# Kernel tuning notes

Measured on AMD Instinct MI355X. Metric: run time of the kernel, lower is better.

Reference implementation:

```python
import jax, jax.numpy as jnp
import numpy as np

NUM_HEADS = 12
HEAD_DIM = 64
SCALE = HEAD_DIM ** -0.5


def setup_inputs() -> dict:
    key = jax.random.key(0)
    ks = jax.random.split(key, 6)
    B, N, C = 32, 577, 768
    x = jax.random.normal(ks[0], (B, N, C), dtype=jnp.float32)
    w_qkv = jax.random.normal(ks[1], (3 * C, C), dtype=jnp.float32) * (C ** -0.5)
    w_proj = jax.random.normal(ks[2], (C, C), dtype=jnp.float32) * (C ** -0.5)
    b_proj = jnp.zeros((C,), dtype=jnp.float32)
    # RoPE tables for the N-1 patch tokens, per rotation pair (head_dim//2)
    ang = jax.random.uniform(ks[3], (N - 1, HEAD_DIM // 2), dtype=jnp.float32) * (2 * np.pi)
    cos = jnp.cos(ang)
    sin = jnp.sin(ang)
    return {"x": x, "w_qkv": w_qkv, "w_proj": w_proj, "b_proj": b_proj, "cos": cos, "sin": sin}


def _rotate(t, cos, sin):
    # t: [B,H,P,D]; cos/sin: [P,D/2] broadcast to [1,1,P,D/2]
    t1 = t[..., 0::2]
    t2 = t[..., 1::2]
    c = cos[None, None]
    s = sin[None, None]
    r1 = t1 * c - t2 * s
    r2 = t1 * s + t2 * c
    return jnp.stack([r1, r2], axis=-1).reshape(t.shape)


def reference(x, w_qkv, w_proj, b_proj, cos, sin):
    B, N, C = x.shape
    H, D = NUM_HEADS, HEAD_DIM
    qkv = (x @ w_qkv.T).reshape(B, N, 3, H, D)
    qkv = jnp.transpose(qkv, (2, 0, 3, 1, 4))  # [3,B,H,N,D]
    q, k, v = qkv[0], qkv[1], qkv[2]
    # RoPE on patch tokens only; CLS token (index 0) left unrotated
    q = jnp.concatenate([q[:, :, :1], _rotate(q[:, :, 1:], cos, sin)], axis=2)
    k = jnp.concatenate([k[:, :, :1], _rotate(k[:, :, 1:], cos, sin)], axis=2)
    attn = jnp.einsum("bhqd,bhkd->bhqk", q, k) * SCALE
    attn = jax.nn.softmax(attn, axis=-1)
    out = jnp.einsum("bhqk,bhkd->bhqd", attn, v)
    out = jnp.transpose(out, (0, 2, 1, 3)).reshape(B, N, C)
    return out @ w_proj.T + b_proj
```

## Files before the change

kernel.cpp:

```cpp
#include <hip/hip_runtime.h>


#define M_ROWS 18464
#define M_PAD  18560
#define CDIM   768
#define QKVN   2304
#define NHEADS 12
#define BHEADS 384
#define NSEQ   577
#define NPAD   640
#define SCALE  0.125f

typedef __bf16 bf16x8 __attribute__((ext_vector_type(8)));
typedef __bf16 bf16x4 __attribute__((ext_vector_type(4)));
typedef float  f32x4  __attribute__((ext_vector_type(4)));

typedef const __attribute__((address_space(1))) void* gas_ptr;
typedef __attribute__((address_space(3))) void* las_ptr;

__device__ inline void gload16(const __bf16* g, __bf16* l) {
  __builtin_amdgcn_global_load_lds((gas_ptr)g, (las_ptr)l, 16, 0, 0);
}

__device__ inline int xcd_swizzle(int orig, int nwg) {
  int q = nwg >> 3, r = nwg & 7;
  int xcd = orig & 7, idx = orig >> 3;
  int base = (xcd < r) ? xcd * (q + 1) : r * (q + 1) + (xcd - r) * q;
  return base + idx;
}


__global__ void cvt_pad(const float* __restrict__ src, __bf16* __restrict__ dst,
                        long n_src, long n_dst) {
  long i = ((long)blockIdx.x * 256 + threadIdx.x) * 4;
  if (i >= n_dst) return;
  if (i + 3 < n_src) {
    f32x4 v = *(const f32x4*)(src + i);
    bf16x4 o = {(__bf16)v[0], (__bf16)v[1], (__bf16)v[2], (__bf16)v[3]};
    *(bf16x4*)(dst + i) = o;
  } else {
#pragma unroll
    for (int j = 0; j < 4; j++)
      if (i + j < n_dst) dst[i + j] = (i + j < n_src) ? (__bf16)src[i + j] : (__bf16)0.0f;
  }
}

__global__ void pad_zero(__bf16* __restrict__ q, __bf16* __restrict__ k) {
  int i = blockIdx.x * 256 + threadIdx.x;
  if (i >= BHEADS * 63 * 64) return;
  int d = i & 63;
  int t = i >> 6;
  int sp = t % 63, bh = t / 63;
  int s = NSEQ + sp;
  q[((size_t)bh * NPAD + s) * 64 + d] = (__bf16)0.0f;
  k[((size_t)bh * NPAD + s) * 64 + d] = (__bf16)0.0f;
}


#define G1_NWG (18 * 145)

__launch_bounds__(256, 2)
__global__ void gemm1(const __bf16* __restrict__ A, const __bf16* __restrict__ Bw,
                      __bf16* __restrict__ qq, __bf16* __restrict__ kk,
                      __bf16* __restrict__ vr,
                      const float* __restrict__ cs, const float* __restrict__ sn) {
  __shared__ __bf16 smem[3 * 4096 * 2];
  const int wgid = xcd_swizzle(blockIdx.x, G1_NWG);
  const int bn = wgid % 18, bm = wgid / 18;
  const int tid = threadIdx.x;
  const int w = tid >> 6, lane = tid & 63;
  const int lr = lane & 15, quad = lane >> 4;
  const int r0 = tid >> 2;
  const int kq = (tid & 3) * 8;
  const int K = CDIM;

  f32x4 acc[4][4] = {};
  const __bf16* Ab = A + (size_t)(bm * 128 + r0) * K + kq;
  const __bf16* Bb = Bw + (size_t)(bn * 128 + r0) * K + kq;
  const int wm = (w >> 1) * 64, wn = (w & 1) * 64;

  auto stage = [&](int kt, int buf) __attribute__((always_inline)) {
    gload16(Ab + kt, &smem[buf * 4096 + tid * 8]);
    gload16(Ab + kt + 64 * K, &smem[buf * 4096 + tid * 8 + 2048]);
    gload16(Bb + kt, &smem[12288 + buf * 4096 + tid * 8]);
    gload16(Bb + kt + 64 * K, &smem[12288 + buf * 4096 + tid * 8 + 2048]);
  };

  stage(0, 0);
  stage(32, 1);
  asm volatile("s_waitcnt vmcnt(4)" ::: "memory");
  asm volatile("s_barrier" ::: "memory");

  int c0 = 0, c1 = 1, c2 = 2;
#pragma unroll 1
  for (int kt = 0; kt < K; kt += 32) {
    if (kt + 64 < K) stage(kt + 64, c2);

    bf16x8 af[4], bfr[4];
#pragma unroll
    for (int i = 0; i < 4; i++) {
      af[i]  = *(const bf16x8*)&smem[c0 * 4096 + (wm + i * 16 + lr) * 32 + quad * 8];
      bfr[i] = *(const bf16x8*)&smem[12288 + c0 * 4096 + (wn + i * 16 + lr) * 32 + quad * 8];
    }
#pragma unroll
    for (int i = 0; i < 4; i++)
#pragma unroll
      for (int j = 0; j < 4; j++)
        acc[i][j] = __builtin_amdgcn_mfma_f32_16x16x32_bf16(af[i], bfr[j], acc[i][j], 0, 0, 0);

    if (kt + 64 < K)      asm volatile("s_waitcnt vmcnt(4)" ::: "memory");
    else if (kt + 32 < K) asm volatile("s_waitcnt vmcnt(0)" ::: "memory");
    asm volatile("s_barrier" ::: "memory");

    int tmp = c0; c0 = c1; c1 = c2; c2 = tmp;
  }

  __syncthreads();
  __bf16* tile = smem;
  const bool isv = (bn >= 12);

#pragma unroll
  for (int i = 0; i < 4; i++) {
#pragma unroll
    for (int r = 0; r < 4; r++) {
      int ml = wm + i * 16 + quad * 4 + r;
      int m = bm * 128 + ml;
      int s = 0;
      if (!isv) { int b = m / NSEQ; s = m - b * NSEQ; }
#pragma unroll
      for (int j = 0; j < 4; j++) {
        int nl = wn + j * 16 + lr;
        float v = acc[i][j][r];
        float outv = v;
        if (!isv) {
          float pv = __shfl_xor(v, 1, 64);
          if (s >= 1 && m < M_ROWS) {
            int d = nl & 63;
            float c  = cs[(size_t)(s - 1) * 32 + (d >> 1)];
            float sv = sn[(size_t)(s - 1) * 32 + (d >> 1)];
            outv = (nl & 1) ? (pv * sv + v * c) : (v * c - pv * sv);
          }
        }
        tile[ml * 136 + nl] = (__bf16)outv;
      }
    }
  }
  __syncthreads();

  {
    const int tq = tid >> 4, tc = tid & 15;
    const int t_blk = bn / 6;
    const int bnq = bn % 6;
    __bf16* dstb = (t_blk == 0) ? qq : (t_blk == 1) ? kk : vr;
    const int SS = (t_blk == 2) ? NSEQ : NPAD;
    const int h = bnq * 2 + (tc >> 3);
    const int d0 = (tc & 7) * 8;
#pragma unroll
    for (int p = 0; p < 8; p++) {
      int ml = p * 16 + tq;
      int m = bm * 128 + ml;
      if (m < M_ROWS) {
        int b = m / NSEQ, s = m - b * NSEQ;
        bf16x8 val = *(const bf16x8*)&tile[ml * 136 + tc * 8];
        *(bf16x8*)&dstb[(((size_t)(b * NHEADS + h) * SS + s) << 6) + d0] = val;
      }
    }
  }
}


__global__ void vtrans(const __bf16* __restrict__ vr, __bf16* __restrict__ vt) {
  __shared__ __bf16 t[64 * 72];
  int blk = blockIdx.x;
  int bh = blk / 10, sc = blk % 10;
  int tid = threadIdx.x;
  int ts = tid >> 2;
  int dc = (tid & 3) * 16;
  int s = sc * 64 + ts;
  bf16x8 a = {}, b2 = {};
  if (s < NSEQ) {
    const __bf16* src = vr + ((size_t)bh * NSEQ + s) * 64 + dc;
    a  = *(const bf16x8*)src;
    b2 = *(const bf16x8*)(src + 8);
  }
#pragma unroll
  for (int e = 0; e < 8; e++) {
    t[(dc + e) * 72 + ts]     = a[e];
    t[(dc + 8 + e) * 72 + ts] = b2[e];
  }
  __syncthreads();
  int d = tid >> 2;
  int scol = (tid & 3) * 16;
  bf16x8 o0 = *(const bf16x8*)&t[d * 72 + scol];
  bf16x8 o1 = *(const bf16x8*)&t[d * 72 + scol + 8];
  __bf16* dst = vt + ((size_t)bh * 64 + d) * NPAD + sc * 64 + scol;
  *(bf16x8*)dst = o0;
  *(bf16x8*)(dst + 8) = o1;
}


#define AT_NWG (BHEADS * 5)

__launch_bounds__(256, 3)
__global__ void attn(const __bf16* __restrict__ q, const __bf16* __restrict__ k,
                     const __bf16* __restrict__ vT, __bf16* __restrict__ aoh) {
  __shared__ __bf16 KVs[2][8192];
  __shared__ float Xf[4][1152];
  const int blk = xcd_swizzle(blockIdx.x, AT_NWG);
  const int qt5 = blk % 5, bh = blk / 5;
  const int b = bh / NHEADS, h = bh % NHEADS;
  const int tid = threadIdx.x;
  const int w = tid >> 6, lane = tid & 63;
  const int lr = lane & 15, quad = lane >> 4;
  const int qbase = qt5 * 128 + w * 32;

  float* xw = &Xf[w][0];
  __bf16* pw = (__bf16*)xw;

  bf16x8 qf[2][2];
#pragma unroll
  for (int qt = 0; qt < 2; qt++)
#pragma unroll
    for (int kh = 0; kh < 2; kh++)
      qf[qt][kh] = *(const bf16x8*)(q + ((size_t)bh * NPAD + qbase + qt * 16 + lr) * 64 + kh * 32 + quad * 8);

  f32x4 O[2][4] = {};
  float l_p[2] = {0.0f, 0.0f};
  const float C1 = SCALE * 1.44269504089f;
  const float C0 = -8.0f * 1.44269504089f;
  const __bf16* kbase = k + (size_t)bh * NPAD * 64;
  const __bf16* vbase = vT + (size_t)bh * 64 * NPAD;

  const int sr0 = tid >> 3, sc0 = tid & 7;
  const int sr1 = (256 + tid) >> 3;
  const int cg0 = sc0 ^ (sr0 & 7);
  const int cg1 = sc0 ^ (sr1 & 7);
  auto stage = [&](int kv0, int buf) __attribute__((always_inline)) {
    gload16(kbase + (size_t)(kv0 + sr0) * 64 + cg0 * 8, &KVs[buf][tid * 8]);
    gload16(kbase + (size_t)(kv0 + sr1) * 64 + cg1 * 8, &KVs[buf][2048 + tid * 8]);
    gload16(vbase + (size_t)sr0 * NPAD + kv0 + cg0 * 8, &KVs[buf][4096 + tid * 8]);
    gload16(vbase + (size_t)sr1 * NPAD + kv0 + cg1 * 8, &KVs[buf][6144 + tid * 8]);
  };

  stage(0, 0);
  asm volatile("s_waitcnt vmcnt(0)" ::: "memory");
  asm volatile("s_barrier" ::: "memory");

  int cur = 0;
#pragma unroll 1
  for (int it = 0; it < 9; it++) {
    if (it < 8) stage((it + 1) * 64, cur ^ 1);

    bf16x8 kf[4][2];
#pragma unroll
    for (int nt = 0; nt < 4; nt++)
#pragma unroll
      for (int kh = 0; kh < 2; kh++)
        kf[nt][kh] = *(const bf16x8*)&KVs[cur][(nt * 16 + lr) * 64 + (((kh * 4 + quad) ^ (lr & 7)) * 8)];

    f32x4 st[2][4];
    __builtin_amdgcn_s_setprio(1);
#pragma unroll
    for (int qt = 0; qt < 2; qt++)
#pragma unroll
      for (int nt = 0; nt < 4; nt++) {
        f32x4 z = {};
        z = __builtin_amdgcn_mfma_f32_16x16x32_bf16(kf[nt][0], qf[qt][0], z, 0, 0, 0);
        z = __builtin_amdgcn_mfma_f32_16x16x32_bf16(kf[nt][1], qf[qt][1], z, 0, 0, 0);
        st[qt][nt] = z;
      }
    __builtin_amdgcn_s_setprio(0);

    bf16x8 vf[4][2];
#pragma unroll
    for (int nt2 = 0; nt2 < 4; nt2++)
#pragma unroll
      for (int kt = 0; kt < 2; kt++)
        vf[nt2][kt] = *(const bf16x8*)&KVs[cur][4096 + (nt2 * 16 + lr) * 64 + (((kt * 4 + quad) ^ (lr & 7)) * 8)];

#pragma unroll
    for (int qt = 0; qt < 2; qt++) {
      float rs = 0.0f;
#pragma unroll
      for (int nt = 0; nt < 4; nt++) {
        f32x4 pv;
#pragma unroll
        for (int r = 0; r < 4; r++)
          pv[r] = __builtin_amdgcn_exp2f(st[qt][nt][r] * C1 + C0);
        rs += pv[0] + pv[1] + pv[2] + pv[3];
        bf16x4 pk = {(__bf16)pv[0], (__bf16)pv[1], (__bf16)pv[2], (__bf16)pv[3]};
        *(bf16x4*)&pw[qt * 1152 + lr * 72 + nt * 16 + quad * 4] = pk;
      }
      l_p[qt] += rs;
    }

    bf16x8 pf[2][2];
#pragma unroll
    for (int qt = 0; qt < 2; qt++)
#pragma unroll
      for (int kt = 0; kt < 2; kt++)
        pf[qt][kt] = *(const bf16x8*)&pw[qt * 1152 + lr * 72 + kt * 32 + quad * 8];

    __builtin_amdgcn_s_setprio(1);
#pragma unroll
    for (int qt = 0; qt < 2; qt++)
#pragma unroll
      for (int nt2 = 0; nt2 < 4; nt2++) {
        O[qt][nt2] = __builtin_amdgcn_mfma_f32_16x16x32_bf16(vf[nt2][0], pf[qt][0], O[qt][nt2], 0, 0, 0);
        O[qt][nt2] = __builtin_amdgcn_mfma_f32_16x16x32_bf16(vf[nt2][1], pf[qt][1], O[qt][nt2], 0, 0, 0);
      }
    __builtin_amdgcn_s_setprio(0);

    asm volatile("s_waitcnt vmcnt(0)" ::: "memory");
    asm volatile("s_barrier" ::: "memory");
    cur ^= 1;
  }

  {
    bf16x8 k5[2];
#pragma unroll
    for (int kh = 0; kh < 2; kh++)
      k5[kh] = *(const bf16x8*)(kbase + (size_t)576 * 64 + kh * 32 + quad * 8);
    float p5[2];
#pragma unroll
    for (int qt = 0; qt < 2; qt++) {
      float s = 0.0f;
#pragma unroll
      for (int kh = 0; kh < 2; kh++)
#pragma unroll
        for (int j = 0; j < 8; j++)
          s += (float)qf[qt][kh][j] * (float)k5[kh][j];
      s += __shfl_xor(s, 16, 64);
      s += __shfl_xor(s, 32, 64);
      p5[qt] = __builtin_amdgcn_exp2f(s * C1 + C0);
      if (quad == 0) l_p[qt] += p5[qt];
    }
#pragma unroll
    for (int nt2 = 0; nt2 < 4; nt2++)
#pragma unroll
      for (int r = 0; r < 4; r++) {
        float vv = (float)vbase[(size_t)(nt2 * 16 + quad * 4 + r) * NPAD + 576];
        O[0][nt2][r] += p5[0] * vv;
        O[1][nt2][r] += p5[1] * vv;
      }
  }

#pragma unroll
  for (int qt = 0; qt < 2; qt++) {
    float lf = l_p[qt];
    lf += __shfl_xor(lf, 16, 64);
    lf += __shfl_xor(lf, 32, 64);
    float inv = 1.0f / lf;
#pragma unroll
    for (int nt2 = 0; nt2 < 4; nt2++) {
      f32x4 t;
#pragma unroll
      for (int r = 0; r < 4; r++) t[r] = O[qt][nt2][r] * inv;
      *(f32x4*)&xw[lr * 68 + nt2 * 16 + quad * 4] = t;
    }
#pragma unroll
    for (int p = 0; p < 4; p++) {
      int lm = p * 4 + quad;
      int s = qbase + qt * 16 + lm;
      if (s < NSEQ) {
        f32x4 t = *(const f32x4*)&xw[lm * 68 + lr * 4];
        bf16x4 hi;
#pragma unroll
        for (int r = 0; r < 4; r++) hi[r] = (__bf16)t[r];
        size_t base = ((size_t)b * NSEQ + s) * CDIM + h * 64 + lr * 4;
        *(bf16x4*)&aoh[base] = hi;
      }
    }
  }
}


#define G2_NWG (6 * 145)

__launch_bounds__(256, 2)
__global__ void gemm2(const __bf16* __restrict__ A, const __bf16* __restrict__ Bw,
                      const float* __restrict__ bias, float* __restrict__ out) {
  __shared__ __bf16 As[3][128 * 32];
  __shared__ __bf16 Bs[3][128 * 32];
  const int wgid = xcd_swizzle(blockIdx.x, G2_NWG);
  const int bn = wgid % 6, bm = wgid / 6;
  const int tid = threadIdx.x;
  const int w = tid >> 6, lane = tid & 63;
  const int lr = lane & 15, quad = lane >> 4;
  const int r0 = tid >> 2;
  const int kq = (tid & 3) * 8;
  const int K = CDIM;

  f32x4 acc[4][4] = {};
  const __bf16* Ab = A + (size_t)(bm * 128 + r0) * K + kq;
  const __bf16* Bb = Bw + (size_t)(bn * 128 + r0) * K + kq;
  const int wm = (w >> 1) * 64, wn = (w & 1) * 64;

  auto stage = [&](int kt, int buf) __attribute__((always_inline)) {
    gload16(Ab + kt, &As[buf][tid * 8]);
    gload16(Ab + kt + 64 * K, &As[buf][tid * 8 + 2048]);
    gload16(Bb + kt, &Bs[buf][tid * 8]);
    gload16(Bb + kt + 64 * K, &Bs[buf][tid * 8 + 2048]);
  };

  stage(0, 0);
  stage(32, 1);
  asm volatile("s_waitcnt vmcnt(4)" ::: "memory");
  asm volatile("s_barrier" ::: "memory");

  int c0 = 0, c1 = 1, c2 = 2;
#pragma unroll 1
  for (int kt = 0; kt < K; kt += 32) {
    if (kt + 64 < K) stage(kt + 64, c2);

    bf16x8 af[4], bfr[4];
#pragma unroll
    for (int i = 0; i < 4; i++) {
      af[i]  = *(const bf16x8*)&As[c0][(wm + i * 16 + lr) * 32 + quad * 8];
      bfr[i] = *(const bf16x8*)&Bs[c0][(wn + i * 16 + lr) * 32 + quad * 8];
    }
#pragma unroll
    for (int i = 0; i < 4; i++)
#pragma unroll
      for (int j = 0; j < 4; j++)
        acc[i][j] = __builtin_amdgcn_mfma_f32_16x16x32_bf16(af[i], bfr[j], acc[i][j], 0, 0, 0);

    if (kt + 64 < K)      asm volatile("s_waitcnt vmcnt(4)" ::: "memory");
    else if (kt + 32 < K) asm volatile("s_waitcnt vmcnt(0)" ::: "memory");
    asm volatile("s_barrier" ::: "memory");

    int tmp = c0; c0 = c1; c1 = c2; c2 = tmp;
  }

#pragma unroll
  for (int i = 0; i < 4; i++)
#pragma unroll
    for (int r = 0; r < 4; r++) {
      int m = bm * 128 + wm + i * 16 + quad * 4 + r;
      if (m < M_ROWS) {
#pragma unroll
        for (int j = 0; j < 4; j++) {
          int n = bn * 128 + wn + j * 16 + lr;
          out[(size_t)m * CDIM + n] = acc[i][j][r] + bias[n];
        }
      }
    }
}


extern "C" void kernel_launch(void* const* d_in, const int* in_sizes, int n_in,
                              void* d_out, int out_size, void* d_ws, size_t ws_size,
                              hipStream_t stream) {
  const float* x      = (const float*)d_in[0];
  const float* w_qkv  = (const float*)d_in[1];
  const float* w_proj = (const float*)d_in[2];
  const float* b_proj = (const float*)d_in[3];
  const float* cosp   = (const float*)d_in[4];
  const float* sinp   = (const float*)d_in[5];
  float* out = (float*)d_out;

  char* ws = (char*)d_ws;
  auto carve = [&](size_t elts) {
    __bf16* p = (__bf16*)ws;
    ws += ((elts * 2 + 255) / 256) * 256;
    return p;
  };
  __bf16* xb    = carve((size_t)M_PAD * CDIM);
  __bf16* wqkvb = carve((size_t)QKVN * CDIM);
  __bf16* wpb   = carve((size_t)CDIM * CDIM);
  __bf16* qq    = carve((size_t)BHEADS * NPAD * 64);
  __bf16* kk    = carve((size_t)BHEADS * NPAD * 64);
  __bf16* vv    = carve((size_t)BHEADS * NPAD * 64);
  __bf16* aoh   = carve((size_t)M_PAD * CDIM);
  __bf16* vr    = aoh;

  cvt_pad<<<((M_PAD * CDIM) / 4 + 255) / 256, 256, 0, stream>>>(x, xb, (long)M_ROWS * CDIM, (long)M_PAD * CDIM);
  cvt_pad<<<((QKVN * CDIM) / 4 + 255) / 256, 256, 0, stream>>>(w_qkv, wqkvb, (long)QKVN * CDIM, (long)QKVN * CDIM);
  cvt_pad<<<((CDIM * CDIM) / 4 + 255) / 256, 256, 0, stream>>>(w_proj, wpb, (long)CDIM * CDIM, (long)CDIM * CDIM);
  pad_zero<<<(BHEADS * 63 * 64 + 255) / 256, 256, 0, stream>>>(qq, kk);
  gemm1<<<G1_NWG, 256, 0, stream>>>(xb, wqkvb, qq, kk, vr, cosp, sinp);
  vtrans<<<BHEADS * 10, 256, 0, stream>>>(vr, vv);
  attn<<<AT_NWG, 256, 0, stream>>>(qq, kk, vv, aoh);
  gemm2<<<G2_NWG, 256, 0, stream>>>(aoh, wpb, b_proj, out);
}
```

Measured before the change: 355.6 us.

## Split attention block into 8 waves each owning 16 query rows

Result: no change. 357.2 us (+0.4%).

```diff
diff --git a/kernel.cpp b/kernel.cpp
--- a/kernel.cpp
+++ b/kernel.cpp
@@ -201,45 +201,39 @@
 
 #define AT_NWG (BHEADS * 5)
 
-__launch_bounds__(256, 3)
+__launch_bounds__(512, 2)
 __global__ void attn(const __bf16* __restrict__ q, const __bf16* __restrict__ k,
                      const __bf16* __restrict__ vT, __bf16* __restrict__ aoh) {
   __shared__ __bf16 KVs[2][8192];
-  __shared__ float Xf[4][1152];
+  __shared__ float Xf[8][1152];
   const int blk = xcd_swizzle(blockIdx.x, AT_NWG);
   const int qt5 = blk % 5, bh = blk / 5;
   const int b = bh / NHEADS, h = bh % NHEADS;
   const int tid = threadIdx.x;
   const int w = tid >> 6, lane = tid & 63;
   const int lr = lane & 15, quad = lane >> 4;
-  const int qbase = qt5 * 128 + w * 32;
+  const int qbase = qt5 * 128 + w * 16;
 
   float* xw = &Xf[w][0];
   __bf16* pw = (__bf16*)xw;
 
-  bf16x8 qf[2][2];
-#pragma unroll
-  for (int qt = 0; qt < 2; qt++)
-#pragma unroll
-    for (int kh = 0; kh < 2; kh++)
-      qf[qt][kh] = *(const bf16x8*)(q + ((size_t)bh * NPAD + qbase + qt * 16 + lr) * 64 + kh * 32 + quad * 8);
-
-  f32x4 O[2][4] = {};
-  float l_p[2] = {0.0f, 0.0f};
+  bf16x8 qf[2];
+#pragma unroll
+  for (int kh = 0; kh < 2; kh++)
+    qf[kh] = *(const bf16x8*)(q + ((size_t)bh * NPAD + qbase + lr) * 64 + kh * 32 + quad * 8);
+
+  f32x4 O[4] = {};
+  float l_p = 0.0f;
   const float C1 = SCALE * 1.44269504089f;
   const float C0 = -8.0f * 1.44269504089f;
   const __bf16* kbase = k + (size_t)bh * NPAD * 64;
   const __bf16* vbase = vT + (size_t)bh * 64 * NPAD;
 
-  const int sr0 = tid >> 3, sc0 = tid & 7;
-  const int sr1 = (256 + tid) >> 3;
-  const int cg0 = sc0 ^ (sr0 & 7);
-  const int cg1 = sc0 ^ (sr1 & 7);
+  const int sr = tid >> 3, sc = tid & 7;
+  const int cg = sc ^ (sr & 7);
   auto stage = [&](int kv0, int buf) __attribute__((always_inline)) {
-    gload16(kbase + (size_t)(kv0 + sr0) * 64 + cg0 * 8, &KVs[buf][tid * 8]);
-    gload16(kbase + (size_t)(kv0 + sr1) * 64 + cg1 * 8, &KVs[buf][2048 + tid * 8]);
-    gload16(vbase + (size_t)sr0 * NPAD + kv0 + cg0 * 8, &KVs[buf][4096 + tid * 8]);
-    gload16(vbase + (size_t)sr1 * NPAD + kv0 + cg1 * 8, &KVs[buf][6144 + tid * 8]);
+    gload16(kbase + (size_t)(kv0 + sr) * 64 + cg * 8, &KVs[buf][tid * 8]);
+    gload16(vbase + (size_t)sr * NPAD + kv0 + cg * 8, &KVs[buf][4096 + tid * 8]);
   };
 
   stage(0, 0);
@@ -258,17 +252,15 @@
       for (int kh = 0; kh < 2; kh++)
         kf[nt][kh] = *(const bf16x8*)&KVs[cur][(nt * 16 + lr) * 64 + (((kh * 4 + quad) ^ (lr & 7)) * 8)];
 
-    f32x4 st[2][4];
+    f32x4 st[4];
     __builtin_amdgcn_s_setprio(1);
 #pragma unroll
-    for (int qt = 0; qt < 2; qt++)
-#pragma unroll
-      for (int nt = 0; nt < 4; nt++) {
-        f32x4 z = {};
-        z = __builtin_amdgcn_mfma_f32_16x16x32_bf16(kf[nt][0], qf[qt][0], z, 0, 0, 0);
-        z = __builtin_amdgcn_mfma_f32_16x16x32_bf16(kf[nt][1], qf[qt][1], z, 0, 0, 0);
-        st[qt][nt] = z;
-      }
+    for (int nt = 0; nt < 4; nt++) {
+      f32x4 z = {};
+      z = __builtin_amdgcn_mfma_f32_16x16x32_bf16(kf[nt][0], qf[0], z, 0, 0, 0);
+      z = __builtin_amdgcn_mfma_f32_16x16x32_bf16(kf[nt][1], qf[1], z, 0, 0, 0);
+      st[nt] = z;
+    }
     __builtin_amdgcn_s_setprio(0);
 
     bf16x8 vf[4][2];
@@ -278,37 +270,32 @@
       for (int kt = 0; kt < 2; kt++)
         vf[nt2][kt] = *(const bf16x8*)&KVs[cur][4096 + (nt2 * 16 + lr) * 64 + (((kt * 4 + quad) ^ (lr & 7)) * 8)];
 
-#pragma unroll
-    for (int qt = 0; qt < 2; qt++) {
+    {
       float rs = 0.0f;
 #pragma unroll
       for (int nt = 0; nt < 4; nt++) {
         f32x4 pv;
 #pragma unroll
         for (int r = 0; r < 4; r++)
-          pv[r] = __builtin_amdgcn_exp2f(st[qt][nt][r] * C1 + C0);
+          pv[r] = __builtin_amdgcn_exp2f(st[nt][r] * C1 + C0);
         rs += pv[0] + pv[1] + pv[2] + pv[3];
         bf16x4 pk = {(__bf16)pv[0], (__bf16)pv[1], (__bf16)pv[2], (__bf16)pv[3]};
-        *(bf16x4*)&pw[qt * 1152 + lr * 72 + nt * 16 + quad * 4] = pk;
-      }
-      l_p[qt] += rs;
-    }
-
-    bf16x8 pf[2][2];
-#pragma unroll
-    for (int qt = 0; qt < 2; qt++)
-#pragma unroll
-      for (int kt = 0; kt < 2; kt++)
-        pf[qt][kt] = *(const bf16x8*)&pw[qt * 1152 + lr * 72 + kt * 32 + quad * 8];
+        *(bf16x4*)&pw[lr * 72 + nt * 16 + quad * 4] = pk;
+      }
+      l_p += rs;
+    }
+
+    bf16x8 pf[2];
+#pragma unroll
+    for (int kt = 0; kt < 2; kt++)
+      pf[kt] = *(const bf16x8*)&pw[lr * 72 + kt * 32 + quad * 8];
 
     __builtin_amdgcn_s_setprio(1);
 #pragma unroll
-    for (int qt = 0; qt < 2; qt++)
-#pragma unroll
-      for (int nt2 = 0; nt2 < 4; nt2++) {
-        O[qt][nt2] = __builtin_amdgcn_mfma_f32_16x16x32_bf16(vf[nt2][0], pf[qt][0], O[qt][nt2], 0, 0, 0);
-        O[qt][nt2] = __builtin_amdgcn_mfma_f32_16x16x32_bf16(vf[nt2][1], pf[qt][1], O[qt][nt2], 0, 0, 0);
-      }
+    for (int nt2 = 0; nt2 < 4; nt2++) {
+      O[nt2] = __builtin_amdgcn_mfma_f32_16x16x32_bf16(vf[nt2][0], pf[0], O[nt2], 0, 0, 0);
+      O[nt2] = __builtin_amdgcn_mfma_f32_16x16x32_bf16(vf[nt2][1], pf[1], O[nt2], 0, 0, 0);
+    }
     __builtin_amdgcn_s_setprio(0);
 
     asm volatile("s_waitcnt vmcnt(0)" ::: "memory");
@@ -321,33 +308,27 @@
 #pragma unroll
     for (int kh = 0; kh < 2; kh++)
       k5[kh] = *(const bf16x8*)(kbase + (size_t)576 * 64 + kh * 32 + quad * 8);
-    float p5[2];
-#pragma unroll
-    for (int qt = 0; qt < 2; qt++) {
-      float s = 0.0f;
-#pragma unroll
-      for (int kh = 0; kh < 2; kh++)
-#pragma unroll
-        for (int j = 0; j < 8; j++)
-          s += (float)qf[qt][kh][j] * (float)k5[kh][j];
-      s += __shfl_xor(s, 16, 64);
-      s += __shfl_xor(s, 32, 64);
-      p5[qt] = __builtin_amdgcn_exp2f(s * C1 + C0);
-      if (quad == 0) l_p[qt] += p5[qt];
-    }
+    float s = 0.0f;
+#pragma unroll
+    for (int kh = 0; kh < 2; kh++)
+#pragma unroll
+      for (int j = 0; j < 8; j++)
+        s += (float)qf[kh][j] * (float)k5[kh][j];
+    s += __shfl_xor(s, 16, 64);
+    s += __shfl_xor(s, 32, 64);
+    float p5 = __builtin_amdgcn_exp2f(s * C1 + C0);
+    if (quad == 0) l_p += p5;
 #pragma unroll
     for (int nt2 = 0; nt2 < 4; nt2++)
 #pragma unroll
       for (int r = 0; r < 4; r++) {
         float vv = (float)vbase[(size_t)(nt2 * 16 + quad * 4 + r) * NPAD + 576];
-        O[0][nt2][r] += p5[0] * vv;
-        O[1][nt2][r] += p5[1] * vv;
-      }
-  }
-
-#pragma unroll
-  for (int qt = 0; qt < 2; qt++) {
-    float lf = l_p[qt];
+        O[nt2][r] += p5 * vv;
+      }
+  }
+
+  {
+    float lf = l_p;
     lf += __shfl_xor(lf, 16, 64);
     lf += __shfl_xor(lf, 32, 64);
     float inv = 1.0f / lf;
@@ -355,13 +336,13 @@
     for (int nt2 = 0; nt2 < 4; nt2++) {
       f32x4 t;
 #pragma unroll
-      for (int r = 0; r < 4; r++) t[r] = O[qt][nt2][r] * inv;
+      for (int r = 0; r < 4; r++) t[r] = O[nt2][r] * inv;
       *(f32x4*)&xw[lr * 68 + nt2 * 16 + quad * 4] = t;
     }
 #pragma unroll
     for (int p = 0; p < 4; p++) {
       int lm = p * 4 + quad;
-      int s = qbase + qt * 16 + lm;
+      int s = qbase + lm;
       if (s < NSEQ) {
         f32x4 t = *(const f32x4*)&xw[lm * 68 + lr * 4];
         bf16x4 hi;
@@ -480,6 +461,6 @@
   pad_zero<<<(BHEADS * 63 * 64 + 255) / 256, 256, 0, stream>>>(qq, kk);
   gemm1<<<G1_NWG, 256, 0, stream>>>(xb, wqkvb, qq, kk, vr, cosp, sinp);
   vtrans<<<BHEADS * 10, 256, 0, stream>>>(vr, vv);
-  attn<<<AT_NWG, 256, 0, stream>>>(qq, kk, vv, aoh);
+  attn<<<AT_NWG, 512, 0, stream>>>(qq, kk, vv, aoh);
   gemm2<<<G2_NWG, 256, 0, stream>>>(aoh, wpb, b_proj, out);
 }
```
